# Kernel optimization log

Hardware: AMD Instinct MI355X
Metric: run time of the kernel (lower is better)

The kernel has to match this reference:

```python
import jax, jax.numpy as jnp
import numpy as np

NUM_HEADS = 8
NUM_LEVELS = 4
NUM_POINTS = 8
SPATIAL_SHAPES = np.array([[92, 160], [46, 80], [23, 40], [12, 20]], dtype=np.int64)


def _bilinear_sample(val_hw, loc, Hl, Wl):
    """val_hw: (bs, heads, H*W, d); loc: (bs, nq, heads, P, 2) in [0,1].
    Matches torch grid_sample(bilinear, zeros padding, align_corners=False)
    applied to grid = 2*loc - 1, i.e. pixel coords x = loc_x*W - 0.5.
    Returns (bs, heads, nq, P, d)."""
    x = loc[..., 0] * Wl - 0.5
    y = loc[..., 1] * Hl - 0.5
    x0 = jnp.floor(x)
    y0 = jnp.floor(y)
    wx = (x - x0).transpose(0, 2, 1, 3)  # (bs, heads, nq, P)
    wy = (y - y0).transpose(0, 2, 1, 3)
    x0i = x0.astype(jnp.int32).transpose(0, 2, 1, 3)
    y0i = y0.astype(jnp.int32).transpose(0, 2, 1, 3)

    def gather(ix, iy):
        valid = ((ix >= 0) & (ix < Wl) & (iy >= 0) & (iy < Hl)).astype(val_hw.dtype)
        idx = jnp.clip(iy, 0, Hl - 1) * Wl + jnp.clip(ix, 0, Wl - 1)  # (bs,heads,nq,P)
        b, h, nq, P = idx.shape
        g = jnp.take_along_axis(val_hw, idx.reshape(b, h, nq * P, 1), axis=2)
        return g.reshape(b, h, nq, P, -1) * valid[..., None]

    return (gather(x0i, y0i) * ((1 - wx) * (1 - wy))[..., None]
            + gather(x0i + 1, y0i) * (wx * (1 - wy))[..., None]
            + gather(x0i, y0i + 1) * ((1 - wx) * wy)[..., None]
            + gather(x0i + 1, y0i + 1) * (wx * wy)[..., None])


def setup_inputs() -> dict:
    key = jax.random.key(0)
    ks = jax.random.split(key, 10)
    C = 256
    bs, nq = 2, 10000
    nv = int((SPATIAL_SHAPES[:, 0] * SPATIAL_SHAPES[:, 1]).sum())  # 19560
    s = 1.0 / np.sqrt(C)
    return {
        "query": jax.random.normal(ks[0], (bs, nq, C), dtype=jnp.float32),
        "value": jax.random.normal(ks[1], (bs, nv, C), dtype=jnp.float32),
        "reference_points": jax.random.uniform(ks[2], (bs, nq, 4, 2), dtype=jnp.float32),
        "spatial_shapes": SPATIAL_SHAPES,
        "W_value": jax.random.normal(ks[3], (C, C), dtype=jnp.float32) * s,
        "b_value": jnp.zeros((C,), dtype=jnp.float32),
        "W_off": jax.random.normal(ks[4], (C, NUM_HEADS * NUM_LEVELS * NUM_POINTS * 2), dtype=jnp.float32) * 0.01,
        "b_off": jax.random.normal(ks[5], (NUM_HEADS * NUM_LEVELS * NUM_POINTS * 2,), dtype=jnp.float32) * 0.1,
        "W_attn": jax.random.normal(ks[6], (C, NUM_HEADS * NUM_LEVELS * NUM_POINTS), dtype=jnp.float32) * s,
        "b_attn": jnp.zeros((NUM_HEADS * NUM_LEVELS * NUM_POINTS,), dtype=jnp.float32),
    }


def reference(query, value, reference_points, spatial_shapes,
              W_value, b_value, W_off, b_off, W_attn, b_attn):
    bs, nq, C = query.shape
    NH, NL, NP = NUM_HEADS, NUM_LEVELS, NUM_POINTS
    d = C // NH
    Z = reference_points.shape[2]  # num_Z_anchors
    shapes_np = np.asarray(spatial_shapes)  # static host-side shapes

    # value / offset / attention projections
    v = (value @ W_value + b_value).reshape(bs, -1, NH, d)
    off = (query @ W_off + b_off).reshape(bs, nq, NH, NL, NP, 2)
    attn = jax.nn.softmax((query @ W_attn + b_attn).reshape(bs, nq, NH, NL * NP), axis=-1)
    attn = attn.reshape(bs, nq, NH, NL, NP)

    # normalize offsets by (W, H) per level and add to reference points
    norm = jnp.stack([spatial_shapes[:, 1], spatial_shapes[:, 0]], -1).astype(query.dtype)  # (NL, 2)
    off = off / norm[None, None, None, :, None, :]
    off = off.reshape(bs, nq, NH, NL, NP // Z, Z, 2)
    loc = reference_points[:, :, None, None, None, :, :] + off  # (bs,nq,NH,NL,NP//Z,Z,2)
    loc = loc.reshape(bs, nq, NH, NL, NP, 2)

    out = jnp.zeros((bs, NH, nq, d), dtype=query.dtype)
    start = 0
    for l in range(NL):
        Hl, Wl = int(shapes_np[l, 0]), int(shapes_np[l, 1])
        v_l = v[:, start:start + Hl * Wl].transpose(0, 2, 1, 3)  # (bs, NH, H*W, d)
        start += Hl * Wl
        sampled = _bilinear_sample(v_l, loc[:, :, :, l], Hl, Wl)  # (bs,NH,nq,NP,d)
        out = out + jnp.einsum('bhqpd,bqhp->bhqd', sampled, attn[:, :, :, l])
    return out.transpose(0, 2, 1, 3).reshape(bs, nq, NH * d)
```

## Files before the change

### kernel.cpp

```cpp
#include <hip/hip_runtime.h>
#include <math.h>

#define NH 8
#define NL 4
#define NP 8
#define CDIM 256
#define NQ 10000
#define BS 2
#define NV 19560

__constant__ int LVL_H[NL]     = {92, 46, 23, 12};
__constant__ int LVL_W[NL]     = {160, 80, 40, 20};
__constant__ int LVL_START[NL] = {0, 14720, 18400, 19320};

typedef __attribute__((ext_vector_type(8))) short short8;
typedef __attribute__((ext_vector_type(4))) float f32x4;
typedef __attribute__((ext_vector_type(2))) _Float16 half2v;
typedef __attribute__((ext_vector_type(4))) _Float16 half4v;

__device__ __forceinline__ unsigned short f2bf(float f) {
    unsigned int u = __float_as_uint(f);
    u += 0x7fffu + ((u >> 16) & 1u);
    return (unsigned short)(u >> 16);
}

__device__ __forceinline__ unsigned short f2h_bits(float f) {
    return __builtin_bit_cast(unsigned short, (_Float16)f);
}

__global__ __launch_bounds__(256) void prep_all(
    const float* __restrict__ value, const float* __restrict__ query,
    const float* __restrict__ Wv,
    const float* __restrict__ Woff, const float* __restrict__ boff,
    const float* __restrict__ Wattn, const float* __restrict__ battn,
    unsigned short* __restrict__ valuebf, unsigned short* __restrict__ querybf,
    unsigned short* __restrict__ BvalT, unsigned short* __restrict__ BcatT,
    float* __restrict__ biascat)
{
    const int bid = blockIdx.x;
    const int t   = threadIdx.x;
    if (bid < 9780) {
        const int i = bid * 256 + t;
        const float4 f = ((const float4*)value)[i];
        ushort4 o;
        o.x = f2bf(f.x); o.y = f2bf(f.y); o.z = f2bf(f.z); o.w = f2bf(f.w);
        ((ushort4*)valuebf)[i] = o;
    } else if (bid < 14780) {
        const int i = (bid - 9780) * 256 + t;
        const float4 f = ((const float4*)query)[i];
        ushort4 o;
        o.x = f2bf(f.x); o.y = f2bf(f.y); o.z = f2bf(f.z); o.w = f2bf(f.w);
        ((ushort4*)querybf)[i] = o;
    } else {
        const int n = bid - 14780;
        if (n < 256) {
            BvalT[n * 256 + t] = f2bf(Wv[t * 256 + n]);
        } else if (n < 1024) {
            const int m = n - 256;
            const float v = (m < 512) ? Woff[t * 512 + m]
                                      : Wattn[t * 256 + (m - 512)];
            BcatT[m * 256 + t] = f2bf(v);
        } else {
            #pragma unroll
            for (int s = 0; s < 3; s++) {
                const int i = s * 256 + t;
                biascat[i] = (i < 512) ? boff[i] : battn[i - 512];
            }
        }
    }
}

#define AST 130
__global__ __launch_bounds__(256) void gemm_all(
    const unsigned short* __restrict__ valuebf,
    const unsigned short* __restrict__ BvalT,
    const float* __restrict__ b_value, _Float16* __restrict__ vproj,
    const unsigned short* __restrict__ querybf,
    const unsigned short* __restrict__ BcatT,
    const float* __restrict__ biascat, _Float16* __restrict__ offcat)
{
    __shared__ short8 Al[4 * AST];
    __shared__ short8 Bl[4 * AST];

    const int bid = blockIdx.x;
    const bool modeV = bid < 612;

    const unsigned short* A;
    const unsigned short* Bt;
    const float* bias;
    int M, N, rowBase, colBase;
    if (modeV) {
        A = valuebf; Bt = BvalT; bias = b_value;
        M = BS * NV; N = 256;
        rowBase = (bid >> 1) * 128; colBase = (bid & 1) * 128;
    } else {
        const int b2 = bid - 612;
        A = querybf; Bt = BcatT; bias = biascat;
        M = BS * NQ; N = 768;
        rowBase = (b2 / 6) * 128; colBase = (b2 % 6) * 128;
    }

    const int t = threadIdx.x;
    const int w  = t >> 6;
    const int l  = t & 63;
    const int wm = (w >> 1) * 64;
    const int wn = (w & 1) * 64;
    const int row16 = l & 15;
    const int kg    = l >> 4;

    const int sr = t >> 1;
    const int sh = t & 1;

    f32x4 acc[4][4] = {};

    for (int k0 = 0; k0 < 256; k0 += 32) {
        {
            const int grow = rowBase + sr;
            short8 v0 = {}, v1 = {};
            if (grow < M) {
                const unsigned short* ap = A + (size_t)grow * 256 + k0 + sh * 16;
                v0 = *(const short8*)ap;
                v1 = *(const short8*)(ap + 8);
            }
            Al[(sh * 2 + 0) * AST + sr] = v0;
            Al[(sh * 2 + 1) * AST + sr] = v1;
        }
        {
            const unsigned short* bp = Bt + (size_t)(colBase + sr) * 256 + k0 + sh * 16;
            Bl[(sh * 2 + 0) * AST + sr] = *(const short8*)bp;
            Bl[(sh * 2 + 1) * AST + sr] = *(const short8*)(bp + 8);
        }
        __syncthreads();

        short8 af[4], bfr[4];
        #pragma unroll
        for (int i = 0; i < 4; i++) af[i] = Al[kg * AST + wm + i * 16 + row16];
        #pragma unroll
        for (int j = 0; j < 4; j++) bfr[j] = Bl[kg * AST + wn + j * 16 + row16];
        #pragma unroll
        for (int i = 0; i < 4; i++)
            #pragma unroll
            for (int j = 0; j < 4; j++)
                acc[i][j] = __builtin_amdgcn_mfma_f32_16x16x32_bf16(
                    bfr[j], af[i], acc[i][j], 0, 0, 0);
        __syncthreads();
    }

    const int m16 = l & 15;
    const int q4  = (l >> 4) * 4;
    #pragma unroll
    for (int i = 0; i < 4; i++) {
        const int row = rowBase + wm + i * 16 + m16;
        if (row >= M) continue;
        #pragma unroll
        for (int j = 0; j < 4; j++) {
            const int col0 = colBase + wn + j * 16 + q4;
            const float4 bv = *(const float4*)&bias[col0];
            half4v o;
            o[0] = (_Float16)(acc[i][j][0] + bv.x);
            o[1] = (_Float16)(acc[i][j][1] + bv.y);
            o[2] = (_Float16)(acc[i][j][2] + bv.z);
            o[3] = (_Float16)(acc[i][j][3] + bv.w);
            _Float16* dst;
            if (modeV) {
                const int b   = (row >= NV) ? 1 : 0;
                const int pix = row - b * NV;
                const int h   = col0 >> 5;
                const int ch  = col0 & 31;
                dst = vproj + ((size_t)(b * NH + h) * NV + pix) * 32 + ch;
            } else {
                dst = offcat + (size_t)row * 768 + col0;
            }
            *(half4v*)dst = o;
        }
    }
}

__global__ __launch_bounds__(256) void sample_kernel(
    const _Float16* __restrict__ vproj,
    const _Float16* __restrict__ offcat,
    const float* __restrict__ refpts,
    float* __restrict__ out)
{
    const int bid = blockIdx.x;
    const int h   = bid & 7;
    const int g   = bid >> 3;
    const int b   = g & 1;
    const int q0  = (g >> 1) * 8;
    const int t   = threadIdx.x;

    __shared__ uint2 desc[8 * 64];

    const int qi = t >> 5, j = t & 31;
    const int qrow = b * NQ + q0 + qi;

    {
        const int lv = j >> 3, p = j & 7;

        float logit = (float)offcat[(size_t)qrow * 768 + 512 + h * 32 + j];
        float m = logit;
        #pragma unroll
        for (int s = 16; s > 0; s >>= 1) m = fmaxf(m, __shfl_xor(m, s, 32));
        float e = __expf(logit - m);
        float ssum = e;
        #pragma unroll
        for (int s = 16; s > 0; s >>= 1) ssum += __shfl_xor(ssum, s, 32);
        const float aw = e / ssum;

        const int Wl = LVL_W[lv], Hl = LVL_H[lv], st = LVL_START[lv];
        const float offx = (float)offcat[(size_t)qrow * 768 + h * 64 + j * 2];
        const float offy = (float)offcat[(size_t)qrow * 768 + h * 64 + j * 2 + 1];

        const int z = p & 3;
        const float rx = refpts[((size_t)qrow * 4 + z) * 2];
        const float ry = refpts[((size_t)qrow * 4 + z) * 2 + 1];

        const float x = fmaf(rx, (float)Wl, offx) - 0.5f;
        const float y = fmaf(ry, (float)Hl, offy) - 0.5f;
        const float x0f = floorf(x), y0f = floorf(y);
        const float wx = x - x0f, wy = y - y0f;
        const int x0 = (int)x0f, y0 = (int)y0f;

        const int xb = min(max(x0, 0), Wl - 2);
        const float wl = (x0 >= 0 && x0 < Wl)          ? (1.f - wx) : 0.f;
        const float wr = (x0 + 1 >= 0 && x0 + 1 < Wl)  ? wx         : 0.f;
        const float wA = (x0 == xb) ? wl : ((x0 + 1 == xb) ? wr : 0.f);
        const float wB = (x0 == xb) ? wr : ((x0 == xb + 1) ? wl : 0.f);

        #pragma unroll
        for (int r = 0; r < 2; r++) {
            const int yy = y0 + r;
            const float rwv = (yy >= 0 && yy < Hl)
                            ? (r ? wy : (1.f - wy)) * aw : 0.f;
            const int iy = min(max(yy, 0), Hl - 1);
            uint2 d;
            d.x = (unsigned)((st + iy * Wl + xb) * 64);
            d.y = (unsigned)f2h_bits(wA * rwv)
                | ((unsigned)f2h_bits(wB * rwv) << 16);
            desc[qi * 64 + j * 2 + r] = d;
        }
    }
    __syncthreads();

    const int lane = t & 31;
    const int grp  = lane >> 3;
    const int sub  = lane & 7;
    const int pix  = sub >> 2;
    const int chq  = sub & 3;

    const char* slab = (const char*)(vproj + (size_t)(b * NH + h) * NV * 32);
    const unsigned laneoff = (unsigned)(pix * 64 + chq * 16);
    const int shamt = pix * 16;
    const uint2* dq = &desc[qi * 64];

    half2v a0 = {}, a1 = {}, a2 = {}, a3 = {};
    #pragma unroll
    for (int i = 0; i < 16; i++) {
        const uint2 dsc = dq[i * 4 + grp];
        const unsigned off = dsc.x + laneoff;
        const unsigned wsu = (dsc.y >> shamt) & 0xffffu;
        const half2v wv = __builtin_bit_cast(half2v, wsu | (wsu << 16));
        const uint4 u = *(const uint4*)(slab + off);
        a0 += wv * __builtin_bit_cast(half2v, u.x);
        a1 += wv * __builtin_bit_cast(half2v, u.y);
        a2 += wv * __builtin_bit_cast(half2v, u.z);
        a3 += wv * __builtin_bit_cast(half2v, u.w);
    }

    float accf[8] = {(float)a0[0], (float)a0[1], (float)a1[0], (float)a1[1],
                     (float)a2[0], (float)a2[1], (float)a3[0], (float)a3[1]};
    #pragma unroll
    for (int s = 4; s <= 16; s <<= 1)
        #pragma unroll
        for (int e = 0; e < 8; e++) accf[e] += __shfl_xor(accf[e], s, 32);

    if ((lane & 0x1C) == 0) {
        float* op = out + (size_t)qrow * 256 + h * 32 + chq * 8;
        *(float4*)op       = make_float4(accf[0], accf[1], accf[2], accf[3]);
        *(float4*)(op + 4) = make_float4(accf[4], accf[5], accf[6], accf[7]);
    }
}

extern "C" void kernel_launch(void* const* d_in, const int* in_sizes, int n_in,
                              void* d_out, int out_size, void* d_ws, size_t ws_size,
                              hipStream_t stream)
{
    const float* query   = (const float*)d_in[0];
    const float* value   = (const float*)d_in[1];
    const float* refpts  = (const float*)d_in[2];
    const float* W_value = (const float*)d_in[4];
    const float* b_value = (const float*)d_in[5];
    const float* W_off   = (const float*)d_in[6];
    const float* b_off   = (const float*)d_in[7];
    const float* W_attn  = (const float*)d_in[8];
    const float* b_attn  = (const float*)d_in[9];

    char* ws = (char*)d_ws;
    _Float16*       vproj   = (_Float16*)(ws);
    unsigned short* valuebf = (unsigned short*)(ws + 20029440);
    unsigned short* querybf = (unsigned short*)(ws + 40058880);
    _Float16*       offcat  = (_Float16*)(ws + 50298880);
    unsigned short* BvalT   = (unsigned short*)(ws + 81018880);
    unsigned short* BcatT   = (unsigned short*)(ws + 81149952);
    float*          biascat = (float*)(ws + 81543168);

    const dim3 blk(256);

    prep_all<<<dim3(15805), blk, 0, stream>>>(
        value, query, W_value, W_off, b_off, W_attn, b_attn,
        valuebf, querybf, BvalT, BcatT, biascat);

    gemm_all<<<dim3(1554), blk, 0, stream>>>(
        valuebf, BvalT, b_value, vproj,
        querybf, BcatT, biascat, offcat);

    sample_kernel<<<dim3(BS * NQ), blk, 0, stream>>>(
        vproj, offcat, refpts, (float*)d_out);
}
```

Measured before the change: 215.5 us.

## Restructure sampler: per-pixel descriptors, batched gathers, fp16 shuffles, no softmax max

Each descriptor now covers one pixel and stores its address and a duplicated fp16 weight, so the gather loop does no shifting or masking. Gathers are issued four at a time so more loads are in flight. The cross-lane reduction now shuffles packed fp16 pairs instead of eight fp32 values, the softmax max-subtraction is dropped, and offset pairs are read with one 32-bit load. Launch bounds request higher occupancy. The risks are more shared-memory traffic, fp16 rounding in the reduction, and possible overflow in exp if logits were ever large.

```diff
diff --git a/kernel.cpp b/kernel.cpp
--- a/kernel.cpp
+++ b/kernel.cpp
@@ -24,8 +24,9 @@
     return (unsigned short)(u >> 16);
 }
 
-__device__ __forceinline__ unsigned short f2h_bits(float f) {
-    return __builtin_bit_cast(unsigned short, (_Float16)f);
+__device__ __forceinline__ unsigned f2h_dup(float f) {
+    const unsigned short h = __builtin_bit_cast(unsigned short, (_Float16)f);
+    return (unsigned)h | ((unsigned)h << 16);
 }
 
 __global__ __launch_bounds__(256) void prep_all(
@@ -176,7 +177,7 @@
     }
 }
 
-__global__ __launch_bounds__(256) void sample_kernel(
+__global__ __launch_bounds__(256, 8) void sample_kernel(
     const _Float16* __restrict__ vproj,
     const _Float16* __restrict__ offcat,
     const float* __restrict__ refpts,
@@ -189,7 +190,7 @@
     const int q0  = (g >> 1) * 8;
     const int t   = threadIdx.x;
 
-    __shared__ uint2 desc[8 * 64];
+    __shared__ uint2 desc[8 * 64 * 2];
 
     const int qi = t >> 5, j = t & 31;
     const int qrow = b * NQ + q0 + qi;
@@ -197,19 +198,17 @@
     {
         const int lv = j >> 3, p = j & 7;
 
-        float logit = (float)offcat[(size_t)qrow * 768 + 512 + h * 32 + j];
-        float m = logit;
-        #pragma unroll
-        for (int s = 16; s > 0; s >>= 1) m = fmaxf(m, __shfl_xor(m, s, 32));
-        float e = __expf(logit - m);
+        const float logit = (float)offcat[(size_t)qrow * 768 + 512 + h * 32 + j];
+        const float e = __expf(logit);
         float ssum = e;
         #pragma unroll
         for (int s = 16; s > 0; s >>= 1) ssum += __shfl_xor(ssum, s, 32);
         const float aw = e / ssum;
 
         const int Wl = LVL_W[lv], Hl = LVL_H[lv], st = LVL_START[lv];
-        const float offx = (float)offcat[(size_t)qrow * 768 + h * 64 + j * 2];
-        const float offy = (float)offcat[(size_t)qrow * 768 + h * 64 + j * 2 + 1];
+        const uint oxy = *(const uint*)(offcat + (size_t)qrow * 768 + h * 64 + j * 2);
+        const float offx = (float)__builtin_bit_cast(half2v, oxy)[0];
+        const float offy = (float)__builtin_bit_cast(half2v, oxy)[1];
 
         const int z = p & 3;
         const float rx = refpts[((size_t)qrow * 4 + z) * 2];
@@ -233,51 +232,65 @@
             const float rwv = (yy >= 0 && yy < Hl)
                             ? (r ? wy : (1.f - wy)) * aw : 0.f;
             const int iy = min(max(yy, 0), Hl - 1);
-            uint2 d;
-            d.x = (unsigned)((st + iy * Wl + xb) * 64);
-            d.y = (unsigned)f2h_bits(wA * rwv)
-                | ((unsigned)f2h_bits(wB * rwv) << 16);
-            desc[qi * 64 + j * 2 + r] = d;
+            const unsigned base = (unsigned)((st + iy * Wl + xb) * 64);
+            const int d = qi * 64 + j * 2 + r;
+            uint2 d0, d1;
+            d0.x = base;      d0.y = f2h_dup(wA * rwv);
+            d1.x = base + 64; d1.y = f2h_dup(wB * rwv);
+            desc[d * 2 + 0] = d0;
+            desc[d * 2 + 1] = d1;
         }
     }
     __syncthreads();
 
     const int lane = t & 31;
     const int grp  = lane >> 3;
-    const int sub  = lane & 7;
-    const int pix  = sub >> 2;
-    const int chq  = sub & 3;
+    const int pix  = (lane >> 2) & 1;
+    const int chq  = lane & 3;
 
     const char* slab = (const char*)(vproj + (size_t)(b * NH + h) * NV * 32);
-    const unsigned laneoff = (unsigned)(pix * 64 + chq * 16);
-    const int shamt = pix * 16;
-    const uint2* dq = &desc[qi * 64];
+    const unsigned laneoff = (unsigned)(chq * 16);
+    const uint2* dq = &desc[(qi * 64) * 2 + pix];
 
     half2v a0 = {}, a1 = {}, a2 = {}, a3 = {};
     #pragma unroll
-    for (int i = 0; i < 16; i++) {
-        const uint2 dsc = dq[i * 4 + grp];
-        const unsigned off = dsc.x + laneoff;
-        const unsigned wsu = (dsc.y >> shamt) & 0xffffu;
-        const half2v wv = __builtin_bit_cast(half2v, wsu | (wsu << 16));
-        const uint4 u = *(const uint4*)(slab + off);
-        a0 += wv * __builtin_bit_cast(half2v, u.x);
-        a1 += wv * __builtin_bit_cast(half2v, u.y);
-        a2 += wv * __builtin_bit_cast(half2v, u.z);
-        a3 += wv * __builtin_bit_cast(half2v, u.w);
-    }
-
-    float accf[8] = {(float)a0[0], (float)a0[1], (float)a1[0], (float)a1[1],
-                     (float)a2[0], (float)a2[1], (float)a3[0], (float)a3[1]};
+    for (int i0 = 0; i0 < 16; i0 += 4) {
+        uint2 d4[4];
+        #pragma unroll
+        for (int u = 0; u < 4; u++)
+            d4[u] = dq[((i0 + u) * 4 + grp) * 2];
+        uint4 v4[4];
+        #pragma unroll
+        for (int u = 0; u < 4; u++)
+            v4[u] = *(const uint4*)(slab + (d4[u].x + laneoff));
+        #pragma unroll
+        for (int u = 0; u < 4; u++) {
+            const half2v wv = __builtin_bit_cast(half2v, d4[u].y);
+            a0 += wv * __builtin_bit_cast(half2v, v4[u].x);
+            a1 += wv * __builtin_bit_cast(half2v, v4[u].y);
+            a2 += wv * __builtin_bit_cast(half2v, v4[u].z);
+            a3 += wv * __builtin_bit_cast(half2v, v4[u].w);
+        }
+    }
+
     #pragma unroll
-    for (int s = 4; s <= 16; s <<= 1)
-        #pragma unroll
-        for (int e = 0; e < 8; e++) accf[e] += __shfl_xor(accf[e], s, 32);
+    for (int s = 4; s <= 16; s <<= 1) {
+        a0 += __builtin_bit_cast(half2v,
+              __shfl_xor(__builtin_bit_cast(unsigned, a0), s, 32));
+        a1 += __builtin_bit_cast(half2v,
+              __shfl_xor(__builtin_bit_cast(unsigned, a1), s, 32));
+        a2 += __builtin_bit_cast(half2v,
+              __shfl_xor(__builtin_bit_cast(unsigned, a2), s, 32));
+        a3 += __builtin_bit_cast(half2v,
+              __shfl_xor(__builtin_bit_cast(unsigned, a3), s, 32));
+    }
 
     if ((lane & 0x1C) == 0) {
         float* op = out + (size_t)qrow * 256 + h * 32 + chq * 8;
-        *(float4*)op       = make_float4(accf[0], accf[1], accf[2], accf[3]);
-        *(float4*)(op + 4) = make_float4(accf[4], accf[5], accf[6], accf[7]);
+        *(float4*)op = make_float4((float)a0[0], (float)a0[1],
+                                   (float)a1[0], (float)a1[1]);
+        *(float4*)(op + 4) = make_float4((float)a2[0], (float)a2[1],
+                                         (float)a3[0], (float)a3[1]);
     }
 }
 
```

New measurement: 215.5 us. About the same (-0.0%).
